# Kernel tuning notes

Measured on AMD Instinct MI355X. Metric: run time of the kernel, lower is better.

Reference implementation:

```python
import jax, jax.numpy as jnp
import numpy as np
import math

D_MODEL = 256
D_HEAD = 64
N_LEVELS = 2
N_HEADS = 8
N_POINTS = 4
SHAPES = [(100, 176), (50, 88)]  # (H, W) per level -> Len_in = 22000


def setup_inputs() -> dict:
    key = jax.random.key(0)
    ks = jax.random.split(key, 8)
    N, Lq = 2, 22000
    Len_in = sum(h * w for h, w in SHAPES)
    query = jax.random.normal(ks[0], (N, Lq, D_MODEL), jnp.float32)
    input_flatten = jax.random.normal(ks[1], (N, Len_in, D_MODEL), jnp.float32)
    input_spatial_shapes = jnp.array(SHAPES, jnp.int32)
    input_level_start_index = jnp.array([0, SHAPES[0][0] * SHAPES[0][1]], jnp.int32)
    # reference points in pixel units (original divides them by offset_normalizer)
    norm = jnp.array([[w, h] for (h, w) in SHAPES], jnp.float32)  # [L,2] as (x=W, y=H)
    reference_points = jax.random.uniform(ks[2], (N, Lq, N_LEVELS, 2), jnp.float32) * norm[None, None]
    xav = lambda k, shp: jax.random.normal(k, shp, jnp.float32) * math.sqrt(2.0 / (shp[0] + shp[1]))
    Wv = xav(ks[3], (D_MODEL, N_HEADS * D_HEAD))
    bv = jnp.zeros((N_HEADS * D_HEAD,), jnp.float32)
    Woff = jax.random.normal(ks[4], (D_MODEL, N_HEADS * N_LEVELS * N_POINTS * 2), jnp.float32) * 0.01
    # grid-init bias exactly as in _reset_parameters
    thetas = jnp.arange(N_HEADS, dtype=jnp.float32) * (2.0 * math.pi / N_HEADS)
    grid = jnp.stack([jnp.cos(thetas), jnp.sin(thetas)], -1)
    grid = grid / jnp.max(jnp.abs(grid), -1, keepdims=True)
    grid = jnp.tile(grid[:, None, None, :], (1, N_LEVELS, N_POINTS, 1))
    grid = grid * jnp.arange(1, N_POINTS + 1, dtype=jnp.float32)[None, None, :, None]
    boff = grid.reshape(-1)
    Wattn = jax.random.normal(ks[5], (D_MODEL, N_HEADS * N_LEVELS * N_POINTS), jnp.float32) * 0.01
    battn = jnp.zeros((N_HEADS * N_LEVELS * N_POINTS,), jnp.float32)
    Wo = xav(ks[6], (N_HEADS * D_HEAD, D_MODEL))
    bo = jnp.zeros((D_MODEL,), jnp.float32)
    return dict(query=query, reference_points=reference_points, input_flatten=input_flatten,
                Wv=Wv, bv=bv, Woff=Woff, boff=boff, Wattn=Wattn, battn=battn, Wo=Wo, bo=bo,
                input_spatial_shapes=input_spatial_shapes,
                input_level_start_index=input_level_start_index)


def ms_deform_core(value, sampling_locations, attention_weights, shapes_np):
    # value: [N, Len_in, H, D]; sampling_locations: [N, Lq, H, L, P, 2] in [0,1]
    # attention_weights: [N, Lq, H, L, P]
    N, _, Hh_, D = value.shape
    Lq = sampling_locations.shape[1]
    P = sampling_locations.shape[4]
    out = jnp.zeros((N, Lq, Hh_, D), value.dtype)
    start = 0
    for lvl, (Hl, Wl) in enumerate(shapes_np):
        Hl, Wl = int(Hl), int(Wl)
        v = value[:, start:start + Hl * Wl]  # [N, Hl*Wl, H, D]
        start += Hl * Wl
        loc = sampling_locations[:, :, :, lvl]  # [N, Lq, H, P, 2]
        # grid_sample align_corners=False convention
        x = loc[..., 0] * Wl - 0.5
        y = loc[..., 1] * Hl - 0.5
        x0 = jnp.floor(x); y0 = jnp.floor(y)
        fx = x - x0; fy = y - y0
        x0i = x0.astype(jnp.int32); y0i = y0.astype(jnp.int32)
        acc = jnp.zeros((N, Lq, P, Hh_, D), value.dtype)
        for dx, dy, w in ((0, 0, (1 - fx) * (1 - fy)), (1, 0, fx * (1 - fy)),
                          (0, 1, (1 - fx) * fy), (1, 1, fx * fy)):
            xi = x0i + dx; yi = y0i + dy
            valid = (xi >= 0) & (xi < Wl) & (yi >= 0) & (yi < Hl)
            idx = jnp.clip(yi, 0, Hl - 1) * Wl + jnp.clip(xi, 0, Wl - 1)  # [N, Lq, H, P]
            idx_t = idx.transpose(0, 1, 3, 2).reshape(N, Lq * P, Hh_, 1)
            g = jnp.take_along_axis(v, idx_t, axis=1).reshape(N, Lq, P, Hh_, D)
            wz = jnp.where(valid, w, 0.0)  # zero padding outside
            acc = acc + g * wz.transpose(0, 1, 3, 2)[..., None]
        out = out + jnp.einsum('nqphd,nqhp->nqhd', acc, attention_weights[:, :, :, lvl])
    return out.reshape(N, Lq, Hh_ * D)


def reference(query, reference_points, input_flatten, Wv, bv, Woff, boff, Wattn, battn, Wo, bo,
              input_spatial_shapes, input_level_start_index):
    shapes_np = np.asarray(input_spatial_shapes)
    N, Lq, _ = query.shape
    value = (input_flatten @ Wv + bv).reshape(N, -1, N_HEADS, D_HEAD)
    off = (query @ Woff + boff).reshape(N, Lq, N_HEADS, N_LEVELS, N_POINTS, 2)
    aw = jax.nn.softmax((query @ Wattn + battn).reshape(N, Lq, N_HEADS, N_LEVELS * N_POINTS), -1)
    aw = aw.reshape(N, Lq, N_HEADS, N_LEVELS, N_POINTS)
    normalizer = jnp.stack([shapes_np[:, 1], shapes_np[:, 0]], -1).astype(jnp.float32)  # [L,2] (W,H)
    loc = (reference_points[:, :, None, :, None, :] + off) / normalizer[None, None, None, :, None, :]
    out = ms_deform_core(value, loc, aw, shapes_np)
    return out @ Wo + bo
```

## Files before the change

### kernel.cpp

```cpp
#include <hip/hip_runtime.h>

#define LQ        22000
#define LEN_IN    22000
#define NB        2

typedef _Float16 half8 __attribute__((ext_vector_type(8)));
typedef _Float16 half4 __attribute__((ext_vector_type(4)));
typedef _Float16 half2 __attribute__((ext_vector_type(2)));
typedef float    floatx4 __attribute__((ext_vector_type(4)));

__device__ __forceinline__ void gload16(const void* g, void* l) {
    __builtin_amdgcn_global_load_lds(
        (const __attribute__((address_space(1))) void*)g,
        (__attribute__((address_space(3))) void*)l, 16, 0, 0);
}

__global__ __launch_bounds__(256) void prep_kernel(
    const float* __restrict__ Wv, const float* __restrict__ Woff,
    const float* __restrict__ Wattn, const float* __restrict__ Wo,
    const float* __restrict__ boff, const float* __restrict__ battn,
    _Float16* __restrict__ WvT, _Float16* __restrict__ WofT,
    _Float16* __restrict__ WoT, float* __restrict__ biascat)
{
    const int i = blockIdx.x * 256 + threadIdx.x;
    if (i < 131072) {
        int k = i >> 9, n = i & 511;
        WvT[n * 256 + k] = (_Float16)Wv[i];
    } else if (i < 163840) {
        int j = i - 131072; int k = j >> 7, n = j & 127;
        WofT[n * 256 + k] = (_Float16)Woff[j];
    } else if (i < 180224) {
        int j = i - 163840; int k = j >> 6, n = j & 63;
        WofT[(128 + n) * 256 + k] = (_Float16)Wattn[j];
    } else if (i < 311296) {
        int j = i - 180224; int k = j >> 8, n = j & 255;
        WoT[n * 512 + k] = (_Float16)Wo[j];
    } else if (i < 311488) {
        int j = i - 311296;
        biascat[j] = (j < 128) ? boff[j] : battn[j - 128];
    }
}

__global__ void f32_to_f16_kernel(const float* __restrict__ src,
                                  _Float16* __restrict__ dst, int n4)
{
    int i = blockIdx.x * blockDim.x + threadIdx.x;
    const int stride = gridDim.x * blockDim.x;
    for (; i < n4; i += stride) {
        float4 v = reinterpret_cast<const float4*>(src)[i];
        half4 h;
        h[0] = (_Float16)v.x; h[1] = (_Float16)v.y;
        h[2] = (_Float16)v.z; h[3] = (_Float16)v.w;
        reinterpret_cast<half4*>(dst)[i] = h;
    }
}

template<int BN, int K, bool OUT_F16>
__global__ __launch_bounds__(256) void gemm_kernel(
    const _Float16* __restrict__ A,
    const _Float16* __restrict__ BT,
    const float* __restrict__ bias,
    void* __restrict__ C,
    int M, int N)
{
    constexpr int FM  = (BN == 128) ? 4 : 2;
    constexpr int BCW = BN / 32;
    __shared__ __align__(16) char smem[(128 + BN) * 128];
    char* sA = smem;
    char* sB = smem + 128 * 128;

    const int t    = threadIdx.x;
    const int w    = t >> 6;
    const int lane = t & 63;
    const int m0   = blockIdx.x * 128;
    const int n0   = blockIdx.y * BN;
    const int wr   = (BN == 128) ? (w >> 1) * 64 : w * 32;
    const int wc   = (BN == 128) ? (w & 1) * 64 : 0;

    const int srow = lane >> 3;
    const int scol = ((lane & 7) ^ srow) << 4;

    floatx4 acc[FM][4] = {};

    for (int it = 0; it < K / 64; ++it) {
        const int k0 = it * 64;
        #pragma unroll
        for (int j = 0; j < 4; ++j) {
            const int c = w * 4 + j;
            gload16((const char*)A + ((size_t)(m0 + c * 8 + srow) * K + k0) * 2 + scol,
                    sA + c * 1024);
        }
        #pragma unroll
        for (int j = 0; j < BCW; ++j) {
            const int c = w * BCW + j;
            gload16((const char*)BT + ((size_t)(n0 + c * 8 + srow) * K + k0) * 2 + scol,
                    sB + c * 1024);
        }
        __syncthreads();

        #pragma unroll
        for (int kb = 0; kb < 2; ++kb) {
            const int kc = kb * 64 + ((lane >> 4) << 4);
            half8 a[FM], b[4];
            #pragma unroll
            for (int fm = 0; fm < FM; ++fm) {
                const int row = wr + fm * 16 + (lane & 15);
                a[fm] = *reinterpret_cast<const half8*>(
                    sA + row * 128 + (kc ^ ((row & 7) << 4)));
            }
            #pragma unroll
            for (int fn = 0; fn < 4; ++fn) {
                const int row = wc + fn * 16 + (lane & 15);
                b[fn] = *reinterpret_cast<const half8*>(
                    sB + row * 128 + (kc ^ ((row & 7) << 4)));
            }
            #pragma unroll
            for (int fm = 0; fm < FM; ++fm)
                #pragma unroll
                for (int fn = 0; fn < 4; ++fn)
                    acc[fm][fn] = __builtin_amdgcn_mfma_f32_16x16x32_f16(
                        a[fm], b[fn], acc[fm][fn], 0, 0, 0);
        }
        __syncthreads();
    }

    const int crow = (lane >> 4) * 4;
    const int ccol = lane & 15;
    #pragma unroll
    for (int fm = 0; fm < FM; ++fm) {
        #pragma unroll
        for (int fn = 0; fn < 4; ++fn) {
            const int col = n0 + wc + fn * 16 + ccol;
            const float bb = bias[col];
            #pragma unroll
            for (int r2 = 0; r2 < 4; ++r2) {
                const int row = m0 + wr + fm * 16 + crow + r2;
                if (row < M) {
                    const float val = acc[fm][fn][r2] + bb;
                    if (OUT_F16)
                        ((_Float16*)C)[(size_t)row * N + col] = (_Float16)val;
                    else
                        ((float*)C)[(size_t)row * N + col] = val;
                }
            }
        }
    }
}

__global__ __launch_bounds__(256) void sampler_kernel(
    const _Float16* __restrict__ value,
    const _Float16* __restrict__ logits,
    const float*    __restrict__ refp,
    _Float16* __restrict__ sampled)
{
    const int t    = threadIdx.x;
    const int wq   = t >> 6;
    const int lane = t & 63;
    const int q    = blockIdx.x * 4 + wq;

    __shared__ __align__(16) int4  s_idx[4][72];
    __shared__ __align__(16) uint4 s_w[4][72];

    {
        const int s = lane;
        const int h = s >> 3;
        const int l = (s >> 2) & 1;
        const int p = s & 3;
        const _Float16* lg = logits + (size_t)q * 192;

        float logit[8];
        float m = -1e30f;
        #pragma unroll
        for (int j = 0; j < 8; ++j) {
            logit[j] = (float)lg[128 + h * 8 + j];
            m = fmaxf(m, logit[j]);
        }
        float den = 0.f;
        #pragma unroll
        for (int j = 0; j < 8; ++j) den += __expf(logit[j] - m);
        const float aw = __expf(logit[l * 4 + p] - m) / den;

        const int Hl = l ? 50 : 100;
        const int Wl = l ? 88 : 176;
        const int st = l ? 17600 : 0;
        const float rx = refp[q * 4 + l * 2 + 0];
        const float ry = refp[q * 4 + l * 2 + 1];
        const float ox = (float)lg[h * 16 + l * 8 + p * 2 + 0];
        const float oy = (float)lg[h * 16 + l * 8 + p * 2 + 1];

        const float x = rx + ox - 0.5f;
        const float y = ry + oy - 0.5f;
        const float x0f = floorf(x), y0f = floorf(y);
        const float fx = x - x0f, fy = y - y0f;
        const int x0 = (int)x0f, y0 = (int)y0f;

        int4  iv;
        uint4 wv;
        #pragma unroll
        for (int c = 0; c < 4; ++c) {
            const int xi = x0 + (c & 1);
            const int yi = y0 + (c >> 1);
            const bool valid = (xi >= 0) & (xi < Wl) & (yi >= 0) & (yi < Hl);
            const float wb = ((c & 1) ? fx : 1.f - fx) * ((c >> 1) ? fy : 1.f - fy);
            const float wz = valid ? wb * aw : 0.f;
            const int xc = min(max(xi, 0), Wl - 1);
            const int yc = min(max(yi, 0), Hl - 1);
            iv[c] = st + yc * Wl + xc;
            union { half2 h2; unsigned int u; } cv;
            cv.h2[0] = (_Float16)wz; cv.h2[1] = cv.h2[0];
            wv[c] = cv.u;
        }
        const int slot = h * 9 + (l * 4 + p);
        s_idx[wq][slot] = iv;
        s_w[wq][slot]   = wv;
    }
    __syncthreads();

    const int h  = lane >> 3;
    const int d8 = (lane & 7) * 8;
    const _Float16* vbase = value + h * 64 + d8;

    half2 acc0 = {0.f16, 0.f16}, acc1 = acc0, acc2 = acc0, acc3 = acc0;
    #pragma unroll
    for (int s8 = 0; s8 < 8; ++s8) {
        const int4  iv = s_idx[wq][h * 9 + s8];
        const uint4 wv = s_w[wq][h * 9 + s8];
        #pragma unroll
        for (int c = 0; c < 4; ++c) {
            const half8 v = *reinterpret_cast<const half8*>(vbase + (size_t)iv[c] * 512);
            union { unsigned int u; half2 h2; } cv; cv.u = wv[c];
            const half2 wh = cv.h2;
            half2 p0; p0[0] = v[0]; p0[1] = v[1];
            half2 p1; p1[0] = v[2]; p1[1] = v[3];
            half2 p2; p2[0] = v[4]; p2[1] = v[5];
            half2 p3; p3[0] = v[6]; p3[1] = v[7];
            acc0 += p0 * wh;
            acc1 += p1 * wh;
            acc2 += p2 * wh;
            acc3 += p3 * wh;
        }
    }
    half8 o;
    o[0] = acc0[0]; o[1] = acc0[1];
    o[2] = acc1[0]; o[3] = acc1[1];
    o[4] = acc2[0]; o[5] = acc2[1];
    o[6] = acc3[0]; o[7] = acc3[1];
    *reinterpret_cast<half8*>(sampled + (size_t)q * 512 + h * 64 + d8) = o;
}

extern "C" void kernel_launch(void* const* d_in, const int* in_sizes, int n_in,
                              void* d_out, int out_size, void* d_ws, size_t ws_size,
                              hipStream_t stream)
{
    const float* query  = (const float*)d_in[0];
    const float* refp   = (const float*)d_in[1];
    const float* inflat = (const float*)d_in[2];
    const float* Wv     = (const float*)d_in[3];
    const float* bv     = (const float*)d_in[4];
    const float* Woff   = (const float*)d_in[5];
    const float* boff   = (const float*)d_in[6];
    const float* Wattn  = (const float*)d_in[7];
    const float* battn  = (const float*)d_in[8];
    const float* Wo     = (const float*)d_in[9];
    const float* bo     = (const float*)d_in[10];
    float* out = (float*)d_out;

    const int M2 = NB * LQ;
    const int MP = 44032;

    char* ws = (char*)d_ws;
    size_t off = 0;
    auto take = [&](size_t bytes) { char* p = ws + off; off = (off + bytes + 255) & ~(size_t)255; return p; };
    _Float16* WvT     = (_Float16*)take(512 * 256 * 2);
    _Float16* WofT    = (_Float16*)take(192 * 256 * 2);
    _Float16* WoT     = (_Float16*)take(256 * 512 * 2);
    float*    biascat = (float*)   take(192 * 4);
    _Float16* buf0    = (_Float16*)take((size_t)MP * 256 * 2);
    _Float16* value   = (_Float16*)take((size_t)M2 * 512 * 2);
    _Float16* logits  = (_Float16*)take((size_t)M2 * 192 * 2);

    prep_kernel<<<(311488 + 255) / 256, 256, 0, stream>>>(
        Wv, Woff, Wattn, Wo, boff, battn, WvT, WofT, WoT, biascat);

    f32_to_f16_kernel<<<2048, 256, 0, stream>>>(query, buf0, M2 * 256 / 4);
    gemm_kernel<64, 256, true><<<dim3(344, 3), 256, 0, stream>>>(
        buf0, WofT, biascat, logits, M2, 192);

    f32_to_f16_kernel<<<2048, 256, 0, stream>>>(inflat, buf0, M2 * 256 / 4);
    gemm_kernel<128, 256, true><<<dim3(344, 4), 256, 0, stream>>>(
        buf0, WvT, bv, value, M2, 512);

    for (int n = 0; n < NB; ++n) {
        sampler_kernel<<<LQ / 4, 256, 0, stream>>>(
            value  + (size_t)n * LEN_IN * 512,
            logits + (size_t)n * LQ * 192,
            refp   + (size_t)n * LQ * 4,
            buf0);
        gemm_kernel<128, 512, false><<<dim3(172, 2), 256, 0, stream>>>(
            buf0, WoT, bo, out + (size_t)n * LQ * 256, LQ, 256);
    }
}
```

Measured before the change: 348.4 us.

## Double-buffer GEMM LDS tiles and use narrower output-projection tiles

The GEMM kernel now keeps two LDS buffers, so it issues the async global-to-LDS loads for the next K tile while the MFMAs run on the current one, and drops one barrier per iteration. The goal is to hide global load latency behind compute. The output-projection GEMM also switches to BN=64 with twice as many blocks, which adds parallelism. The cost is double the LDS use, which can lower occupancy.

```diff
diff --git a/kernel.cpp b/kernel.cpp
--- a/kernel.cpp
+++ b/kernel.cpp
@@ -65,9 +65,12 @@
 {
     constexpr int FM  = (BN == 128) ? 4 : 2;
     constexpr int BCW = BN / 32;
-    __shared__ __align__(16) char smem[(128 + BN) * 128];
-    char* sA = smem;
-    char* sB = smem + 128 * 128;
+    constexpr int NT  = K / 64;
+
+    __shared__ __align__(16) char sA0[128 * 128];
+    __shared__ __align__(16) char sB0[BN * 128];
+    __shared__ __align__(16) char sA1[128 * 128];
+    __shared__ __align__(16) char sB1[BN * 128];
 
     const int t    = threadIdx.x;
     const int w    = t >> 6;
@@ -82,22 +85,22 @@
 
     floatx4 acc[FM][4] = {};
 
-    for (int it = 0; it < K / 64; ++it) {
-        const int k0 = it * 64;
+    auto stage = [&](char* dA, char* dB, int k0) {
         #pragma unroll
         for (int j = 0; j < 4; ++j) {
             const int c = w * 4 + j;
             gload16((const char*)A + ((size_t)(m0 + c * 8 + srow) * K + k0) * 2 + scol,
-                    sA + c * 1024);
+                    dA + c * 1024);
         }
         #pragma unroll
         for (int j = 0; j < BCW; ++j) {
             const int c = w * BCW + j;
             gload16((const char*)BT + ((size_t)(n0 + c * 8 + srow) * K + k0) * 2 + scol,
-                    sB + c * 1024);
-        }
-        __syncthreads();
-
+                    dB + c * 1024);
+        }
+    };
+
+    auto compute = [&](const char* cA, const char* cB) {
         #pragma unroll
         for (int kb = 0; kb < 2; ++kb) {
             const int kc = kb * 64 + ((lane >> 4) << 4);
@@ -106,13 +109,13 @@
             for (int fm = 0; fm < FM; ++fm) {
                 const int row = wr + fm * 16 + (lane & 15);
                 a[fm] = *reinterpret_cast<const half8*>(
-                    sA + row * 128 + (kc ^ ((row & 7) << 4)));
+                    cA + row * 128 + (kc ^ ((row & 7) << 4)));
             }
             #pragma unroll
             for (int fn = 0; fn < 4; ++fn) {
                 const int row = wc + fn * 16 + (lane & 15);
                 b[fn] = *reinterpret_cast<const half8*>(
-                    sB + row * 128 + (kc ^ ((row & 7) << 4)));
+                    cB + row * 128 + (kc ^ ((row & 7) << 4)));
             }
             #pragma unroll
             for (int fm = 0; fm < FM; ++fm)
@@ -121,6 +124,18 @@
                     acc[fm][fn] = __builtin_amdgcn_mfma_f32_16x16x32_f16(
                         a[fm], b[fn], acc[fm][fn], 0, 0, 0);
         }
+    };
+
+    stage(sA0, sB0, 0);
+    __syncthreads();
+    #pragma unroll
+    for (int it = 0; it < NT; ++it) {
+        char* cA = (it & 1) ? sA1 : sA0;
+        char* cB = (it & 1) ? sB1 : sB0;
+        char* nA = (it & 1) ? sA0 : sA1;
+        char* nB = (it & 1) ? sB0 : sB1;
+        if (it + 1 < NT) stage(nA, nB, (it + 1) * 64);
+        compute(cA, cB);
         __syncthreads();
     }
 
@@ -296,7 +311,7 @@
             logits + (size_t)n * LQ * 192,
             refp   + (size_t)n * LQ * 4,
             buf0);
-        gemm_kernel<128, 512, false><<<dim3(172, 2), 256, 0, stream>>>(
+        gemm_kernel<64, 512, false><<<dim3(172, 4), 256, 0, stream>>>(
             buf0, WoT, bo, out + (size_t)n * LQ * 256, LQ, 256);
     }
 }
```

Result: no change. 352.6 us (+1.2%).

## Merge per-batch launches, fuse input conversions, and swizzle GEMM block order

Applied to the files above, without the earlier changes.

Both f32-to-f16 conversions now run in one kernel writing to separate buffers. The per-batch sampler and output GEMM loops are collapsed into single launches over both batches, with the sampler computing its batch offset from the query index. GEMMs now use a 1D grid remapped with an XCD-style swizzle, so consecutive blocks on one chiplet share A/B tiles. Together these cut launch count and tail effects and improve L2 locality, at the cost of an extra conversion buffer in the workspace.

```diff
diff --git a/kernel.cpp b/kernel.cpp
--- a/kernel.cpp
+++ b/kernel.cpp
@@ -41,17 +41,21 @@
     }
 }
 
-__global__ void f32_to_f16_kernel(const float* __restrict__ src,
-                                  _Float16* __restrict__ dst, int n4)
+__global__ void cvt2_kernel(const float* __restrict__ qsrc,
+                            const float* __restrict__ xsrc,
+                            _Float16* __restrict__ qdst,
+                            _Float16* __restrict__ xdst, int n4)
 {
     int i = blockIdx.x * blockDim.x + threadIdx.x;
     const int stride = gridDim.x * blockDim.x;
-    for (; i < n4; i += stride) {
-        float4 v = reinterpret_cast<const float4*>(src)[i];
+    for (; i < 2 * n4; i += stride) {
+        const bool second = (i >= n4);
+        const int j = second ? i - n4 : i;
+        const float4 v = reinterpret_cast<const float4*>(second ? xsrc : qsrc)[j];
         half4 h;
         h[0] = (_Float16)v.x; h[1] = (_Float16)v.y;
         h[2] = (_Float16)v.z; h[3] = (_Float16)v.w;
-        reinterpret_cast<half4*>(dst)[i] = h;
+        reinterpret_cast<half4*>(second ? xdst : qdst)[j] = h;
     }
 }
 
@@ -61,19 +65,22 @@
     const _Float16* __restrict__ BT,
     const float* __restrict__ bias,
     void* __restrict__ C,
-    int M, int N)
+    int M, int N, int NBY)
 {
     constexpr int FM  = (BN == 128) ? 4 : 2;
     constexpr int BCW = BN / 32;
-    __shared__ __align__(16) char smem[(128 + BN) * 128];
-    char* sA = smem;
-    char* sB = smem + 128 * 128;
+
+    __shared__ __align__(16) char sA[128 * 128];
+    __shared__ __align__(16) char sB[BN * 128];
+
+    const int f  = blockIdx.x;
+    const int nn = (f & 7) * (gridDim.x >> 3) + (f >> 3);
+    const int m0 = (nn / NBY) * 128;
+    const int n0 = (nn % NBY) * BN;
 
     const int t    = threadIdx.x;
     const int w    = t >> 6;
     const int lane = t & 63;
-    const int m0   = blockIdx.x * 128;
-    const int n0   = blockIdx.y * BN;
     const int wr   = (BN == 128) ? (w >> 1) * 64 : w * 32;
     const int wc   = (BN == 128) ? (w & 1) * 64 : 0;
 
@@ -218,7 +225,7 @@
 
     const int h  = lane >> 3;
     const int d8 = (lane & 7) * 8;
-    const _Float16* vbase = value + h * 64 + d8;
+    const _Float16* vbase = value + ((size_t)(q / LQ) * LEN_IN) * 512 + h * 64 + d8;
 
     half2 acc0 = {0.f16, 0.f16}, acc1 = acc0, acc2 = acc0, acc3 = acc0;
     #pragma unroll
@@ -266,7 +273,6 @@
     float* out = (float*)d_out;
 
     const int M2 = NB * LQ;
-    const int MP = 44032;
 
     char* ws = (char*)d_ws;
     size_t off = 0;
@@ -275,28 +281,24 @@
     _Float16* WofT    = (_Float16*)take(192 * 256 * 2);
     _Float16* WoT     = (_Float16*)take(256 * 512 * 2);
     float*    biascat = (float*)   take(192 * 4);
-    _Float16* buf0    = (_Float16*)take((size_t)MP * 256 * 2);
+    _Float16* qbf     = (_Float16*)take((size_t)44032 * 256 * 2);
+    _Float16* inbf    = (_Float16*)take((size_t)44032 * 256 * 2);
     _Float16* value   = (_Float16*)take((size_t)M2 * 512 * 2);
     _Float16* logits  = (_Float16*)take((size_t)M2 * 192 * 2);
+    _Float16* sampled = qbf;
 
     prep_kernel<<<(311488 + 255) / 256, 256, 0, stream>>>(
         Wv, Woff, Wattn, Wo, boff, battn, WvT, WofT, WoT, biascat);
 
-    f32_to_f16_kernel<<<2048, 256, 0, stream>>>(query, buf0, M2 * 256 / 4);
-    gemm_kernel<64, 256, true><<<dim3(344, 3), 256, 0, stream>>>(
-        buf0, WofT, biascat, logits, M2, 192);
-
-    f32_to_f16_kernel<<<2048, 256, 0, stream>>>(inflat, buf0, M2 * 256 / 4);
-    gemm_kernel<128, 256, true><<<dim3(344, 4), 256, 0, stream>>>(
-        buf0, WvT, bv, value, M2, 512);
-
-    for (int n = 0; n < NB; ++n) {
-        sampler_kernel<<<LQ / 4, 256, 0, stream>>>(
-            value  + (size_t)n * LEN_IN * 512,
-            logits + (size_t)n * LQ * 192,
-            refp   + (size_t)n * LQ * 4,
-            buf0);
-        gemm_kernel<128, 512, false><<<dim3(172, 2), 256, 0, stream>>>(
-            buf0, WoT, bo, out + (size_t)n * LQ * 256, LQ, 256);
-    }
-}
+    cvt2_kernel<<<2048, 256, 0, stream>>>(query, inflat, qbf, inbf, M2 * 256 / 4);
+
+    gemm_kernel<128, 256, true><<<344 * 4, 256, 0, stream>>>(
+        inbf, WvT, bv, value, M2, 512, 4);
+    gemm_kernel<64, 256, true><<<344 * 3, 256, 0, stream>>>(
+        qbf, WofT, biascat, logits, M2, 192, 3);
+
+    sampler_kernel<<<M2 / 4, 256, 0, stream>>>(value, logits, refp, sampled);
+
+    gemm_kernel<128, 512, false><<<344 * 2, 256, 0, stream>>>(
+        sampled, WoT, bo, out, M2, 256, 2);
+}
```

Measured after the change: 338.2 us. -2.9%, faster.
